# Optimization experiments

Measured on AMD Instinct MI355X. Metric: run time of the kernel, lower is better.

The kernel has to match this reference:

```python
import jax, jax.numpy as jnp
import numpy as np

EPS = 1e-8

def div_safe(n, d):
    return n / jnp.maximum(d, EPS)

def cos_sim(v1, v2):
    # torch F.cosine_similarity along last axis (broadcasting allowed)
    n1 = jnp.linalg.norm(v1, axis=-1)
    n2 = jnp.linalg.norm(v2, axis=-1)
    dot = jnp.sum(v1 * v2, axis=-1)
    return dot / (jnp.maximum(n1, EPS) * jnp.maximum(n2, EPS))

def cosine_pairwise(v1, v2):
    # v1: (B,L1,H), v2: (B,L2,H) -> (B,L1,L2)
    n1 = jnp.linalg.norm(v1, axis=2)[:, :, None]        # (B,L1,1)
    n2 = jnp.linalg.norm(v2, axis=2)[:, None, :]        # (B,1,L2)
    a = jnp.einsum('bih,bjh->bij', v1, v2)
    return div_safe(a, n1 * n2)

def mpm(v1, v2, w):
    # v1: (B,L,H); v2: (B,L,H) or (B,1,H) (broadcast); w: (P,H)
    mv1 = cos_sim(v1, v2)[..., None]                     # (B,L,1)
    v1w = w[None, None] * v1[:, :, None, :]              # (B,L,P,H)
    v2w = w[None, None] * v2[:, :, None, :]              # (B,L or 1,P,H)
    mvp = cos_sim(v1w, v2w)                              # (B,L,P)
    return [mv1, mvp]

def mpm_pairwise(v1, v2, w):
    # v1: (B,L1,H), v2: (B,L2,H), w: (P,H) -> (B,L1,L2,P)
    v1w = w[None, :, None, :] * v1[:, None, :, :]        # (B,P,L1,H)
    v2w = w[None, :, None, :] * v2[:, None, :, :]        # (B,P,L2,H)
    n = jnp.einsum('bpih,bpjh->bpij', v1w, v2w)
    n1 = jnp.linalg.norm(v1w, axis=3)[:, :, :, None]     # (B,P,L1,1)
    n2 = jnp.linalg.norm(v2w, axis=3)[:, :, None, :]     # (B,P,1,L2)
    return div_safe(n, n1 * n2).transpose(0, 2, 3, 1)

def matching_forward(context_p, mask_p, context_h, mask_h, params):
    H = params.shape[-1]
    B = context_p.shape[0]
    p_fw, p_bw = context_p[..., :H], context_p[..., H:]
    h_fw, h_bw = context_h[..., :H], context_h[..., H:]

    len_p = jnp.sum(mask_p, axis=1)
    len_h = jnp.sum(mask_h, axis=1)
    last_p = jnp.clip(len_p - 1, 0)
    last_h = jnp.clip(len_h - 1, 0)
    bidx = jnp.arange(B)
    p_fw_last = p_fw[bidx, last_p][:, None, :]           # (B,1,H)
    h_fw_last = h_fw[bidx, last_h][:, None, :]
    p_bw_last = p_bw[:, 0:1, :]
    h_bw_last = h_bw[:, 0:1, :]

    cos_fw = cosine_pairwise(p_fw, h_fw)                 # (B,L1,L2)
    cos_bw = cosine_pairwise(p_bw, h_bw)

    mv_p = [cos_fw.max(axis=2, keepdims=True), cos_fw.mean(axis=2, keepdims=True),
            cos_bw.max(axis=2, keepdims=True), cos_bw.mean(axis=2, keepdims=True)]
    mv_h = [cos_fw.max(axis=1)[..., None], cos_fw.mean(axis=1)[..., None],
            cos_bw.max(axis=1)[..., None], cos_bw.mean(axis=1)[..., None]]

    # full match
    mv_p += mpm(p_fw, h_fw_last, params[0]) + mpm(p_bw, h_bw_last, params[1])
    mv_h += mpm(h_fw, p_fw_last, params[0]) + mpm(h_bw, p_bw_last, params[1])

    # maxpool match
    m_fw = mpm_pairwise(p_fw, h_fw, params[2])           # (B,L1,L2,P)
    m_bw = mpm_pairwise(p_bw, h_bw, params[3])
    mv_p += [m_fw.max(axis=2), m_fw.mean(axis=2), m_bw.max(axis=2), m_bw.mean(axis=2)]
    mv_h += [m_fw.max(axis=1), m_fw.mean(axis=1), m_bw.max(axis=1), m_bw.mean(axis=1)]

    # attentive (mean) match -- sum over seq axis expressed as einsum, no 4D tensor
    att_mean_h_fw = div_safe(jnp.einsum('bij,bjh->bih', cos_fw, h_fw), cos_fw.sum(axis=2, keepdims=True))
    att_mean_h_bw = div_safe(jnp.einsum('bij,bjh->bih', cos_bw, h_bw), cos_bw.sum(axis=2, keepdims=True))
    att_mean_p_fw = div_safe(jnp.einsum('bij,bih->bjh', cos_fw, p_fw), cos_fw.sum(axis=1)[..., None])
    att_mean_p_bw = div_safe(jnp.einsum('bij,bih->bjh', cos_bw, p_bw), cos_bw.sum(axis=1)[..., None])
    mv_p += mpm(p_fw, att_mean_h_fw, params[4]) + mpm(p_bw, att_mean_h_bw, params[5])
    mv_h += mpm(h_fw, att_mean_p_fw, params[4]) + mpm(h_bw, att_mean_p_bw, params[5])

    # max-attentive match -- needs elementwise max over the pair axis
    att_max_h_fw = jnp.max(h_fw[:, None, :, :] * cos_fw[..., None], axis=2)  # (B,L1,H)
    att_max_h_bw = jnp.max(h_bw[:, None, :, :] * cos_bw[..., None], axis=2)
    att_max_p_fw = jnp.max(p_fw[:, :, None, :] * cos_fw[..., None], axis=1)  # (B,L2,H)
    att_max_p_bw = jnp.max(p_bw[:, :, None, :] * cos_bw[..., None], axis=1)
    mv_p += mpm(p_fw, att_max_h_fw, params[6]) + mpm(p_bw, att_max_h_bw, params[7])
    mv_h += mpm(h_fw, att_max_p_fw, params[6]) + mpm(h_bw, att_max_p_bw, params[7])

    return jnp.concatenate(mv_p, axis=2), jnp.concatenate(mv_h, axis=2)

def setup_inputs() -> dict:
    key = jax.random.key(0)
    k1, k2, k3 = jax.random.split(key, 3)
    B, L, H, P, M = 16, 128, 100, 20, 8
    context_p = jax.random.normal(k1, (B, L, 2 * H), dtype=jnp.float32)
    context_h = jax.random.normal(k2, (B, L, 2 * H), dtype=jnp.float32)
    mask_p = jnp.ones((B, L), dtype=jnp.int32)
    mask_h = jnp.ones((B, L), dtype=jnp.int32)
    # kaiming_normal_ (fan_in=H): std = sqrt(2/H)
    params = jax.random.normal(k3, (M, P, H), dtype=jnp.float32) * np.sqrt(2.0 / H)
    return {"context_p": context_p, "mask_p": mask_p,
            "context_h": context_h, "mask_h": mask_h, "params": params}

def reference(context_p, mask_p, context_h, mask_h, params):
    return matching_forward(context_p, mask_p, context_h, mask_h, params)
```

## Files before the change

kernel.cpp:

```cpp
#include <hip/hip_runtime.h>
#include <math.h>

#define B 16
#define L 128
#define H 100
#define P 20
#define CH 210
#define EPSF 1e-8f

#define OFF_COS    0u
#define OFF_COST   524288u
#define OFF_ROWSUM 1048576u
#define OFF_COLSUM 1052672u
#define OFF_LASTV  1056768u
#define OFF_W2T    1063168u
#define OFF_W2F    1079968u
#define OFF_NBUF   1101472u
#define OFF_ATT    1273504u

typedef __attribute__((ext_vector_type(8))) short bf16x8;
typedef __attribute__((ext_vector_type(4))) float f32x4;

__device__ inline unsigned short f2bf(float x) {
    union { float f; unsigned u; } c; c.f = x;
    unsigned r = c.u + 0x7fffu + ((c.u >> 16) & 1u);
    return (unsigned short)(r >> 16);
}

__global__ __launch_bounds__(128) void prep_kernel(
    const float* __restrict__ ctx_p, const int* __restrict__ mask_p,
    const float* __restrict__ ctx_h, const int* __restrict__ mask_h,
    float* __restrict__ lastv)
{
    const int b = blockIdx.x, is_h = blockIdx.y, t = threadIdx.x;
    const float* ctx = is_h ? ctx_h : ctx_p;
    const int* mask = is_h ? mask_h : mask_p;
    __shared__ int sm[L];
    sm[t] = mask[b*L + t];
    __syncthreads();
    for (int s = 64; s > 0; s >>= 1) {
        if (t < s) sm[t] += sm[t + s];
        __syncthreads();
    }
    int last = sm[0] - 1;
    if (last < 0) last = 0;
    if (t < H) {
        lastv[((size_t)(is_h*2 + 0)*B + b)*H + t] = ctx[(size_t)(b*L + last)*(2*H) + t];
        lastv[((size_t)(is_h*2 + 1)*B + b)*H + t] = ctx[(size_t)(b*L + 0)*(2*H) + H + t];
    }
}

__global__ __launch_bounds__(256) void wprep_kernel(
    const float* __restrict__ params, float* __restrict__ w2t, float* __restrict__ w2f)
{
    int e = blockIdx.x*256 + threadIdx.x;
    if (e < 8*25*4*21) {
        int m = e / 2100, r = e % 2100;
        int g = r / 84, q = r % 84, hh = q / 21, p = q % 21;
        int h = 4*g + hh;
        float v = 1.f;
        if (p < P) { float w = params[((size_t)m*P + p)*H + h]; v = w*w; }
        w2t[e] = v;
    }
    int e2 = e - 16800;
    if (e2 >= 0 && e2 < 8*21*128) {
        int m = e2 / (21*128), r = e2 % (21*128), p = r / 128, h = r % 128;
        float v = 0.f;
        if (h < H) {
            if (p < P) { float w = params[((size_t)m*P + p)*H + h]; v = w*w; }
            else v = 1.f;
        }
        w2f[e2] = v;
    }
}

__global__ __launch_bounds__(128) void norm_kernel(
    const float* __restrict__ ctx_p, const float* __restrict__ ctx_h,
    const float* __restrict__ w2t, float* __restrict__ nbuf)
{
    const int b = blockIdx.x, dir = blockIdx.y, side = blockIdx.z;
    const int i = threadIdx.x;
    const float* row = (side ? ctx_h : ctx_p) + (size_t)(b*L + i)*(2*H) + dir*H;
    const float* wt = w2t + (size_t)(2 + dir)*2100;
    float n2[21];
#pragma unroll
    for (int p = 0; p < 21; ++p) n2[p] = 0.f;
    for (int g = 0; g < 25; ++g) {
        float4 v = *(const float4*)(row + 4*g);
        float sq[4] = {v.x*v.x, v.y*v.y, v.z*v.z, v.w*v.w};
        const float* wg = wt + g*84;
#pragma unroll
        for (int hh = 0; hh < 4; ++hh)
#pragma unroll
            for (int p = 0; p < 21; ++p)
                n2[p] = fmaf(wg[hh*21 + p], sq[hh], n2[p]);
    }
    float* nb = nbuf + ((size_t)((dir*2 + side)*B + b)*21)*128;
#pragma unroll
    for (int p = 0; p < 21; ++p) nb[p*128 + i] = sqrtf(n2[p]);
}

__global__ __launch_bounds__(256, 2) void pair_kernel(
    const float* __restrict__ ctx_p, const float* __restrict__ ctx_h,
    const float* __restrict__ w2f, const float* __restrict__ nbuf,
    float* __restrict__ cosbuf, float* __restrict__ cosT,
    float* __restrict__ rowsum, float* __restrict__ colsum,
    float* __restrict__ out)
{
    const int b = blockIdx.x, dir = blockIdx.y, p = blockIdx.z;
    const int t = threadIdx.x;
    __shared__ short sB[2048*8];
    __shared__ float colred[2][4][128];

    for (int e = t; e < 2048; e += 256) {
        int cg = e >> 8, kt = (e >> 6) & 3, qq = (e >> 4) & 3, rl2 = e & 15;
        int row = cg*16 + rl2, kb = kt*32 + qq*8;
        float v[8];
#pragma unroll
        for (int j = 0; j < 8; ++j) v[j] = 0.f;
        const float* src = ctx_h + (size_t)(b*L + row)*(2*H) + dir*H;
        if (kb < H)     { float4 f = *(const float4*)(src + kb);     v[0]=f.x; v[1]=f.y; v[2]=f.z; v[3]=f.w; }
        if (kb + 4 < H) { float4 f = *(const float4*)(src + kb + 4); v[4]=f.x; v[5]=f.y; v[6]=f.z; v[7]=f.w; }
        bf16x8 pk;
#pragma unroll
        for (int j = 0; j < 8; ++j) pk[j] = (short)f2bf(v[j]);
        *(bf16x8*)&sB[e*8] = pk;
    }

    const int w = t >> 6, lane = t & 63, q = lane >> 4, rl = lane & 15;
    const float* w2row = w2f + ((size_t)(2 + dir)*21 + p)*128;
    bf16x8 af[2][4];
#pragma unroll
    for (int rgi = 0; rgi < 2; ++rgi) {
        int row = (w*2 + rgi)*16 + rl;
        const float* src = ctx_p + (size_t)(b*L + row)*(2*H) + dir*H;
#pragma unroll
        for (int kt = 0; kt < 4; ++kt) {
            int kb = kt*32 + q*8;
            float v[8];
#pragma unroll
            for (int j = 0; j < 8; ++j) v[j] = 0.f;
            if (kb < H) {
                float4 f = *(const float4*)(src + kb);
                float4 wv = *(const float4*)(w2row + kb);
                v[0]=f.x*wv.x; v[1]=f.y*wv.y; v[2]=f.z*wv.z; v[3]=f.w*wv.w;
            }
            if (kb + 4 < H) {
                float4 f = *(const float4*)(src + kb + 4);
                float4 wv = *(const float4*)(w2row + kb + 4);
                v[4]=f.x*wv.x; v[5]=f.y*wv.y; v[6]=f.z*wv.z; v[7]=f.w*wv.w;
            }
            bf16x8 pk;
#pragma unroll
            for (int j = 0; j < 8; ++j) pk[j] = (short)f2bf(v[j]);
            af[rgi][kt] = pk;
        }
    }
    __syncthreads();

    f32x4 acc[2][8];
#pragma unroll
    for (int rgi = 0; rgi < 2; ++rgi)
#pragma unroll
        for (int cg = 0; cg < 8; ++cg) acc[rgi][cg] = (f32x4)0.f;
#pragma unroll
    for (int kt = 0; kt < 4; ++kt) {
#pragma unroll
        for (int cg = 0; cg < 8; ++cg) {
            bf16x8 bfr = *(bf16x8*)&sB[((cg*4 + kt)*64 + lane)*8];
            acc[0][cg] = __builtin_amdgcn_mfma_f32_16x16x32_bf16(af[0][kt], bfr, acc[0][cg], 0, 0, 0);
            acc[1][cg] = __builtin_amdgcn_mfma_f32_16x16x32_bf16(af[1][kt], bfr, acc[1][cg], 0, 0, 0);
        }
    }

    const float* nbA = nbuf + (((size_t)(dir*2 + 0)*B + b)*21 + p)*128;
    const float* nbB = nbuf + (((size_t)(dir*2 + 1)*B + b)*21 + p)*128;
    float na[2][4];
#pragma unroll
    for (int rgi = 0; rgi < 2; ++rgi)
#pragma unroll
        for (int r = 0; r < 4; ++r) na[rgi][r] = nbA[(w*2 + rgi)*16 + q*4 + r];
    float nbv[8];
#pragma unroll
    for (int cg = 0; cg < 8; ++cg) nbv[cg] = nbB[cg*16 + rl];

    const bool iscos = (p == P);
    float* cosm  = cosbuf + (size_t)(dir*B + b)*16384;
    float* cosmT = cosT   + (size_t)(dir*B + b)*16384;

    int chmax, chmean;
    if (p < P) { chmax = (dir ? 86 : 46) + p; chmean = (dir ? 106 : 66) + p; }
    else       { chmax = dir*2;              chmean = dir*2 + 1; }

    float rowm[2][4], rows_[2][4], colm[8], cols_[8];
#pragma unroll
    for (int rgi = 0; rgi < 2; ++rgi)
#pragma unroll
        for (int r = 0; r < 4; ++r) { rowm[rgi][r] = -INFINITY; rows_[rgi][r] = 0.f; }
#pragma unroll
    for (int cg = 0; cg < 8; ++cg) { colm[cg] = -INFINITY; cols_[cg] = 0.f; }

#pragma unroll
    for (int rgi = 0; rgi < 2; ++rgi) {
        int i0 = (w*2 + rgi)*16 + q*4;
#pragma unroll
        for (int cg = 0; cg < 8; ++cg) {
            float m[4];
#pragma unroll
            for (int r = 0; r < 4; ++r) {
                float d = fmaxf(na[rgi][r]*nbv[cg], EPSF);
                m[r] = acc[rgi][cg][r] * __builtin_amdgcn_rcpf(d);
                rowm[rgi][r] = fmaxf(rowm[rgi][r], m[r]);
                rows_[rgi][r] += m[r];
            }
            float cM = fmaxf(fmaxf(m[0], m[1]), fmaxf(m[2], m[3]));
            colm[cg] = fmaxf(colm[cg], cM);
            cols_[cg] += (m[0] + m[1]) + (m[2] + m[3]);
            if (iscos) {
                int j = cg*16 + rl;
                float4 f4; f4.x = m[0]; f4.y = m[1]; f4.z = m[2]; f4.w = m[3];
                *(float4*)&cosmT[j*128 + i0] = f4;
#pragma unroll
                for (int r = 0; r < 4; ++r) cosm[(i0 + r)*128 + j] = m[r];
            }
        }
    }
#pragma unroll
    for (int rgi = 0; rgi < 2; ++rgi)
#pragma unroll
        for (int r = 0; r < 4; ++r) {
            float mx = rowm[rgi][r], sm = rows_[rgi][r];
#pragma unroll
            for (int d = 1; d < 16; d <<= 1) {
                mx = fmaxf(mx, __shfl_xor(mx, d));
                sm += __shfl_xor(sm, d);
            }
            if (rl == 0) {
                int i = (w*2 + rgi)*16 + q*4 + r;
                float* orow = out + (size_t)(b*L + i)*CH;
                orow[chmax] = mx; orow[chmean] = sm * (1.f/L);
                if (iscos) rowsum[(dir*B + b)*L + i] = sm;
            }
        }
#pragma unroll
    for (int cg = 0; cg < 8; ++cg) {
        float mx = colm[cg], sm = cols_[cg];
        mx = fmaxf(mx, __shfl_xor(mx, 16)); sm += __shfl_xor(sm, 16);
        mx = fmaxf(mx, __shfl_xor(mx, 32)); sm += __shfl_xor(sm, 32);
        if (q == 0) { colred[0][w][cg*16 + rl] = mx; colred[1][w][cg*16 + rl] = sm; }
    }
    __syncthreads();
    {
        int c = t & 127, kind = t >> 7;
        float v0 = colred[kind][0][c], v1 = colred[kind][1][c];
        float v2 = colred[kind][2][c], v3 = colred[kind][3][c];
        float* oh = out + (size_t)B*L*CH + (size_t)(b*L + c)*CH;
        if (kind == 0) {
            oh[chmax] = fmaxf(fmaxf(v0, v1), fmaxf(v2, v3));
        } else {
            float sm = (v0 + v1) + (v2 + v3);
            oh[chmean] = sm * (1.f/L);
            if (iscos) colsum[(dir*B + b)*L + c] = sm;
        }
    }
}

__global__ __launch_bounds__(256) void att_kernel(
    const float* __restrict__ ctx_p, const float* __restrict__ ctx_h,
    const float* __restrict__ cosbuf, const float* __restrict__ cosT,
    const float* __restrict__ rowsum, const float* __restrict__ colsum,
    float* __restrict__ attbuf)
{
    const int b = blockIdx.x;
    const int dir = blockIdx.y >> 1, side = blockIdx.y & 1;
    const int rc = blockIdx.z, r0 = rc*16;
    const int t = threadIdx.x;

    __shared__ float sv[L][H];
    __shared__ float cvT[L][16];

    const float* mat = (side ? cosbuf : cosT) + (size_t)(dir*B + b)*16384;
    const float* src = side ? ctx_p : ctx_h;

    for (int e = t; e < 3200; e += 256) {
        int row = e / 25, g = e - row*25;
        *(float4*)&sv[row][4*g] =
            *(const float4*)(src + (size_t)(b*L + row)*(2*H) + dir*H + 4*g);
    }
    for (int e = t; e < 2048; e += 256) {
        int s = e >> 4, r = e & 15;
        cvT[s][r] = mat[s*L + r0 + r];
    }
    __syncthreads();

    const int tr = t & 7, th = t >> 3;
    if (th < 25) {
        float acc[2][4], amx[2][4];
#pragma unroll
        for (int rr = 0; rr < 2; ++rr)
#pragma unroll
            for (int qq = 0; qq < 4; ++qq) { acc[rr][qq] = 0.f; amx[rr][qq] = -INFINITY; }
        for (int s = 0; s < L; ++s) {
            float2 c2 = *(const float2*)&cvT[s][2*tr];
            float4 v4 = *(const float4*)&sv[s][4*th];
            float cs[2] = {c2.x, c2.y};
            float vs[4] = {v4.x, v4.y, v4.z, v4.w};
#pragma unroll
            for (int rr = 0; rr < 2; ++rr)
#pragma unroll
                for (int qq = 0; qq < 4; ++qq) {
                    float pr = cs[rr] * vs[qq];
                    acc[rr][qq] += pr;
                    amx[rr][qq] = fmaxf(amx[rr][qq], pr);
                }
        }
        const float* den = side ? colsum : rowsum;
#pragma unroll
        for (int rr = 0; rr < 2; ++rr) {
            int rg = r0 + 2*tr + rr;
            float d = fmaxf(den[(dir*B + b)*L + rg], EPSF);
            float* meanp = attbuf + ((((size_t)side*2 + 0)*2 + dir)*B*L + (b*L + rg))*H + 4*th;
            float* maxp  = attbuf + ((((size_t)side*2 + 1)*2 + dir)*B*L + (b*L + rg))*H + 4*th;
            float4 fm; fm.x = acc[rr][0]/d; fm.y = acc[rr][1]/d; fm.z = acc[rr][2]/d; fm.w = acc[rr][3]/d;
            float4 fx; fx.x = amx[rr][0]; fx.y = amx[rr][1]; fx.z = amx[rr][2]; fx.w = amx[rr][3];
            *(float4*)meanp = fm;
            *(float4*)maxp  = fx;
        }
    }
}

__global__ __launch_bounds__(128) void point_kernel(
    const float* __restrict__ ctx_p, const float* __restrict__ ctx_h,
    const float* __restrict__ w2t,
    const float* __restrict__ lastv, const float* __restrict__ attbuf,
    float* __restrict__ out)
{
    const int b = blockIdx.x, side = blockIdx.y;
    const int m = blockIdx.z >> 1, ih = blockIdx.z & 1;
    const int t = threadIdx.x;
    const int il = t & 63, half = t >> 6;
    const int i = ih*64 + il;
    const int dir = m & 1;
    const int wsel_[6] = {0, 1, 4, 5, 6, 7};
    const int chb_[6]  = {4, 25, 126, 147, 168, 189};

    const float* v1p = (side ? ctx_h : ctx_p) + (size_t)(b*L + i)*(2*H) + dir*H;
    const float* v2p;
    if (m < 2) {
        v2p = lastv + ((size_t)((side ? 0 : 2) + dir)*B + b)*H;
    } else {
        int kind = (m >= 4) ? 1 : 0;
        v2p = attbuf + ((((size_t)side*2 + kind)*2 + dir)*B*L + (b*L + i))*H;
    }
    const float* wt = w2t + (size_t)wsel_[m]*2100;

    float s11[21], s22[21], s12[21];
#pragma unroll
    for (int p = 0; p < 21; ++p) { s11[p] = 0.f; s22[p] = 0.f; s12[p] = 0.f; }
    const int g0 = half ? 13 : 0, g1 = half ? 25 : 13;
    for (int g = g0; g < g1; ++g) {
        float4 x = *(const float4*)(v1p + 4*g);
        float4 y = *(const float4*)(v2p + 4*g);
        float xx[4] = {x.x*x.x, x.y*x.y, x.z*x.z, x.w*x.w};
        float yy[4] = {y.x*y.x, y.y*y.y, y.z*y.z, y.w*y.w};
        float xy[4] = {x.x*y.x, x.y*y.y, x.z*y.z, x.w*y.w};
        const float* wg = wt + g*84;
#pragma unroll
        for (int hh = 0; hh < 4; ++hh)
#pragma unroll
            for (int p = 0; p < 21; ++p) {
                float w2 = wg[hh*21 + p];
                s11[p] = fmaf(w2, xx[hh], s11[p]);
                s22[p] = fmaf(w2, yy[hh], s22[p]);
                s12[p] = fmaf(w2, xy[hh], s12[p]);
            }
    }
    __shared__ float red[3][21][64];
    if (half) {
#pragma unroll
        for (int p = 0; p < 21; ++p) {
            red[0][p][il] = s11[p]; red[1][p][il] = s22[p]; red[2][p][il] = s12[p];
        }
    }
    __syncthreads();
    if (!half) {
        float* orow = out + (size_t)side*B*L*CH + (size_t)(b*L + i)*CH;
#pragma unroll
        for (int p = 0; p < 21; ++p) {
            float a = s11[p] + red[0][p][il];
            float c = s22[p] + red[1][p][il];
            float d = s12[p] + red[2][p][il];
            float cv = d / (fmaxf(sqrtf(a), EPSF) * fmaxf(sqrtf(c), EPSF));
            orow[(p == P) ? chb_[m] : (chb_[m] + 1 + p)] = cv;
        }
    }
}

extern "C" void kernel_launch(void* const* d_in, const int* in_sizes, int n_in,
                              void* d_out, int out_size, void* d_ws, size_t ws_size,
                              hipStream_t stream) {
    const float* ctx_p  = (const float*)d_in[0];
    const int*   mask_p = (const int*)d_in[1];
    const float* ctx_h  = (const float*)d_in[2];
    const int*   mask_h = (const int*)d_in[3];
    const float* params = (const float*)d_in[4];
    float* out = (float*)d_out;

    float* ws = (float*)d_ws;
    float* cosbuf = ws + OFF_COS;
    float* cosT   = ws + OFF_COST;
    float* rowsum = ws + OFF_ROWSUM;
    float* colsum = ws + OFF_COLSUM;
    float* lastv  = ws + OFF_LASTV;
    float* w2t    = ws + OFF_W2T;
    float* w2f    = ws + OFF_W2F;
    float* nbuf   = ws + OFF_NBUF;
    float* attbuf = ws + OFF_ATT;

    prep_kernel <<<dim3(B, 2),     128, 0, stream>>>(ctx_p, mask_p, ctx_h, mask_h, lastv);
    wprep_kernel<<<dim3(150),      256, 0, stream>>>(params, w2t, w2f);
    norm_kernel <<<dim3(B, 2, 2),  128, 0, stream>>>(ctx_p, ctx_h, w2t, nbuf);
    pair_kernel <<<dim3(B, 2, 21), 256, 0, stream>>>(ctx_p, ctx_h, w2f, nbuf,
                                                     cosbuf, cosT, rowsum, colsum, out);
    att_kernel  <<<dim3(B, 4, 8),  256, 0, stream>>>(ctx_p, ctx_h, cosbuf, cosT,
                                                     rowsum, colsum, attbuf);
    point_kernel<<<dim3(B, 2, 12), 128, 0, stream>>>(ctx_p, ctx_h, w2t, lastv, attbuf, out);
}
```

Before: 148.8 us.

## Fuse prep, weight-prep and norm kernels into pair kernel

Removes three small preliminary launches. Their work now runs inside the pair kernel: extra blocks build w2t and the last-token vectors, and each pair block computes its own weighted row norms into LDS straight from params. This cuts launch overhead and the serial dependency chain, plus the w2f and nbuf round trips through global memory. In exchange the norm work is repeated per block, adding a 100-element loop per thread before the MFMA stage.

```diff
diff --git a/kernel.cpp b/kernel.cpp
--- a/kernel.cpp
+++ b/kernel.cpp
@@ -14,9 +14,7 @@
 #define OFF_COLSUM 1052672u
 #define OFF_LASTV  1056768u
 #define OFF_W2T    1063168u
-#define OFF_W2F    1079968u
-#define OFF_NBUF   1101472u
-#define OFF_ATT    1273504u
+#define OFF_ATT    1079968u
 
 typedef __attribute__((ext_vector_type(8))) short bf16x8;
 typedef __attribute__((ext_vector_type(4))) float f32x4;
@@ -27,94 +25,57 @@
     return (unsigned short)(r >> 16);
 }
 
-__global__ __launch_bounds__(128) void prep_kernel(
-    const float* __restrict__ ctx_p, const int* __restrict__ mask_p,
-    const float* __restrict__ ctx_h, const int* __restrict__ mask_h,
-    float* __restrict__ lastv)
-{
-    const int b = blockIdx.x, is_h = blockIdx.y, t = threadIdx.x;
-    const float* ctx = is_h ? ctx_h : ctx_p;
-    const int* mask = is_h ? mask_h : mask_p;
-    __shared__ int sm[L];
-    sm[t] = mask[b*L + t];
-    __syncthreads();
-    for (int s = 64; s > 0; s >>= 1) {
-        if (t < s) sm[t] += sm[t + s];
-        __syncthreads();
-    }
-    int last = sm[0] - 1;
-    if (last < 0) last = 0;
-    if (t < H) {
-        lastv[((size_t)(is_h*2 + 0)*B + b)*H + t] = ctx[(size_t)(b*L + last)*(2*H) + t];
-        lastv[((size_t)(is_h*2 + 1)*B + b)*H + t] = ctx[(size_t)(b*L + 0)*(2*H) + H + t];
-    }
-}
-
-__global__ __launch_bounds__(256) void wprep_kernel(
-    const float* __restrict__ params, float* __restrict__ w2t, float* __restrict__ w2f)
-{
-    int e = blockIdx.x*256 + threadIdx.x;
-    if (e < 8*25*4*21) {
-        int m = e / 2100, r = e % 2100;
-        int g = r / 84, q = r % 84, hh = q / 21, p = q % 21;
-        int h = 4*g + hh;
-        float v = 1.f;
-        if (p < P) { float w = params[((size_t)m*P + p)*H + h]; v = w*w; }
-        w2t[e] = v;
-    }
-    int e2 = e - 16800;
-    if (e2 >= 0 && e2 < 8*21*128) {
-        int m = e2 / (21*128), r = e2 % (21*128), p = r / 128, h = r % 128;
-        float v = 0.f;
-        if (h < H) {
-            if (p < P) { float w = params[((size_t)m*P + p)*H + h]; v = w*w; }
-            else v = 1.f;
-        }
-        w2f[e2] = v;
-    }
-}
-
-__global__ __launch_bounds__(128) void norm_kernel(
-    const float* __restrict__ ctx_p, const float* __restrict__ ctx_h,
-    const float* __restrict__ w2t, float* __restrict__ nbuf)
-{
-    const int b = blockIdx.x, dir = blockIdx.y, side = blockIdx.z;
-    const int i = threadIdx.x;
-    const float* row = (side ? ctx_h : ctx_p) + (size_t)(b*L + i)*(2*H) + dir*H;
-    const float* wt = w2t + (size_t)(2 + dir)*2100;
-    float n2[21];
-#pragma unroll
-    for (int p = 0; p < 21; ++p) n2[p] = 0.f;
-    for (int g = 0; g < 25; ++g) {
-        float4 v = *(const float4*)(row + 4*g);
-        float sq[4] = {v.x*v.x, v.y*v.y, v.z*v.z, v.w*v.w};
-        const float* wg = wt + g*84;
-#pragma unroll
-        for (int hh = 0; hh < 4; ++hh)
-#pragma unroll
-            for (int p = 0; p < 21; ++p)
-                n2[p] = fmaf(wg[hh*21 + p], sq[hh], n2[p]);
-    }
-    float* nb = nbuf + ((size_t)((dir*2 + side)*B + b)*21)*128;
-#pragma unroll
-    for (int p = 0; p < 21; ++p) nb[p*128 + i] = sqrtf(n2[p]);
-}
-
 __global__ __launch_bounds__(256, 2) void pair_kernel(
     const float* __restrict__ ctx_p, const float* __restrict__ ctx_h,
-    const float* __restrict__ w2f, const float* __restrict__ nbuf,
+    const int* __restrict__ mask_p, const int* __restrict__ mask_h,
+    const float* __restrict__ params,
     float* __restrict__ cosbuf, float* __restrict__ cosT,
     float* __restrict__ rowsum, float* __restrict__ colsum,
+    float* __restrict__ lastv, float* __restrict__ w2t,
     float* __restrict__ out)
 {
-    const int b = blockIdx.x, dir = blockIdx.y, p = blockIdx.z;
-    const int t = threadIdx.x;
-    __shared__ short sB[2048*8];
-    __shared__ float colred[2][4][128];
+    __shared__ __align__(16) char smem[37888];
+    const int k = blockIdx.x, t = threadIdx.x;
+
+    if (k >= 672) {
+        if (k == 672) {
+            for (int e = t; e < 16800; e += 256) {
+                int m = e / 2100, r = e % 2100;
+                int g = r / 84, qq = r % 84, hh = qq / 21, p = qq % 21;
+                int h = 4*g + hh;
+                float v = 1.f;
+                if (p < P) { float w = params[((size_t)m*P + p)*H + h]; v = w*w; }
+                w2t[e] = v;
+            }
+        } else {
+            const int task = k - 673, b = task >> 1, is_h = task & 1;
+            const float* ctx = is_h ? ctx_h : ctx_p;
+            const int* mask = is_h ? mask_h : mask_p;
+            int* sm = (int*)smem;
+            if (t < 128) sm[t] = mask[b*L + t];
+            __syncthreads();
+            for (int s = 64; s > 0; s >>= 1) {
+                if (t < s) sm[t] += sm[t + s];
+                __syncthreads();
+            }
+            int last = sm[0] - 1;
+            if (last < 0) last = 0;
+            if (t < H) {
+                lastv[((size_t)(is_h*2 + 0)*B + b)*H + t] = ctx[(size_t)(b*L + last)*(2*H) + t];
+                lastv[((size_t)(is_h*2 + 1)*B + b)*H + t] = ctx[(size_t)(b*L + 0)*(2*H) + H + t];
+            }
+        }
+        return;
+    }
+
+    const int b = k & 15, dir = (k >> 4) & 1, p = k >> 5;
+    short* sB     = (short*)smem;
+    float* colred = (float*)(smem + 32768);
+    float* nlds   = (float*)(smem + 32768 + 4096);
 
     for (int e = t; e < 2048; e += 256) {
-        int cg = e >> 8, kt = (e >> 6) & 3, qq = (e >> 4) & 3, rl2 = e & 15;
-        int row = cg*16 + rl2, kb = kt*32 + qq*8;
+        int cgi = e >> 8, kt = (e >> 6) & 3, qq = (e >> 4) & 3, rl2 = e & 15;
+        int row = cgi*16 + rl2, kb = kt*32 + qq*8;
         float v[8];
 #pragma unroll
         for (int j = 0; j < 8; ++j) v[j] = 0.f;
@@ -127,8 +88,9 @@
         *(bf16x8*)&sB[e*8] = pk;
     }
 
+    const float* prow = params + ((size_t)(2 + dir)*P + p)*H;
+
     const int w = t >> 6, lane = t & 63, q = lane >> 4, rl = lane & 15;
-    const float* w2row = w2f + ((size_t)(2 + dir)*21 + p)*128;
     bf16x8 af[2][4];
 #pragma unroll
     for (int rgi = 0; rgi < 2; ++rgi) {
@@ -140,15 +102,20 @@
             float v[8];
 #pragma unroll
             for (int j = 0; j < 8; ++j) v[j] = 0.f;
-            if (kb < H) {
-                float4 f = *(const float4*)(src + kb);
-                float4 wv = *(const float4*)(w2row + kb);
-                v[0]=f.x*wv.x; v[1]=f.y*wv.y; v[2]=f.z*wv.z; v[3]=f.w*wv.w;
-            }
-            if (kb + 4 < H) {
-                float4 f = *(const float4*)(src + kb + 4);
-                float4 wv = *(const float4*)(w2row + kb + 4);
-                v[4]=f.x*wv.x; v[5]=f.y*wv.y; v[6]=f.z*wv.z; v[7]=f.w*wv.w;
+            if (p < P) {
+                if (kb < H) {
+                    float4 f = *(const float4*)(src + kb);
+                    float4 wv = *(const float4*)(prow + kb);
+                    v[0]=f.x*wv.x*wv.x; v[1]=f.y*wv.y*wv.y; v[2]=f.z*wv.z*wv.z; v[3]=f.w*wv.w*wv.w;
+                }
+                if (kb + 4 < H) {
+                    float4 f = *(const float4*)(src + kb + 4);
+                    float4 wv = *(const float4*)(prow + kb + 4);
+                    v[4]=f.x*wv.x*wv.x; v[5]=f.y*wv.y*wv.y; v[6]=f.z*wv.z*wv.z; v[7]=f.w*wv.w*wv.w;
+                }
+            } else {
+                if (kb < H)     { float4 f = *(const float4*)(src + kb);     v[0]=f.x; v[1]=f.y; v[2]=f.z; v[3]=f.w; }
+                if (kb + 4 < H) { float4 f = *(const float4*)(src + kb + 4); v[4]=f.x; v[5]=f.y; v[6]=f.z; v[7]=f.w; }
             }
             bf16x8 pk;
 #pragma unroll
@@ -156,33 +123,54 @@
             af[rgi][kt] = pk;
         }
     }
+
+    {
+        const int r = t & 127, sd = t >> 7;
+        const float* nrow = (sd ? ctx_h : ctx_p) + (size_t)(b*L + r)*(2*H) + dir*H;
+        float n2 = 0.f;
+        if (p < P) {
+            for (int g = 0; g < 25; ++g) {
+                float4 v = *(const float4*)(nrow + 4*g);
+                float4 wv = *(const float4*)(prow + 4*g);
+                n2 = fmaf(wv.x*wv.x, v.x*v.x, n2);
+                n2 = fmaf(wv.y*wv.y, v.y*v.y, n2);
+                n2 = fmaf(wv.z*wv.z, v.z*v.z, n2);
+                n2 = fmaf(wv.w*wv.w, v.w*v.w, n2);
+            }
+        } else {
+            for (int g = 0; g < 25; ++g) {
+                float4 v = *(const float4*)(nrow + 4*g);
+                n2 = fmaf(v.x, v.x, n2); n2 = fmaf(v.y, v.y, n2);
+                n2 = fmaf(v.z, v.z, n2); n2 = fmaf(v.w, v.w, n2);
+            }
+        }
+        nlds[sd*128 + r] = sqrtf(n2);
+    }
     __syncthreads();
 
     f32x4 acc[2][8];
 #pragma unroll
     for (int rgi = 0; rgi < 2; ++rgi)
 #pragma unroll
-        for (int cg = 0; cg < 8; ++cg) acc[rgi][cg] = (f32x4)0.f;
+        for (int cgi = 0; cgi < 8; ++cgi) acc[rgi][cgi] = (f32x4)0.f;
 #pragma unroll
     for (int kt = 0; kt < 4; ++kt) {
 #pragma unroll
-        for (int cg = 0; cg < 8; ++cg) {
-            bf16x8 bfr = *(bf16x8*)&sB[((cg*4 + kt)*64 + lane)*8];
-            acc[0][cg] = __builtin_amdgcn_mfma_f32_16x16x32_bf16(af[0][kt], bfr, acc[0][cg], 0, 0, 0);
-            acc[1][cg] = __builtin_amdgcn_mfma_f32_16x16x32_bf16(af[1][kt], bfr, acc[1][cg], 0, 0, 0);
-        }
-    }
-
-    const float* nbA = nbuf + (((size_t)(dir*2 + 0)*B + b)*21 + p)*128;
-    const float* nbB = nbuf + (((size_t)(dir*2 + 1)*B + b)*21 + p)*128;
+        for (int cgi = 0; cgi < 8; ++cgi) {
+            bf16x8 bfr = *(bf16x8*)&sB[((cgi*4 + kt)*64 + lane)*8];
+            acc[0][cgi] = __builtin_amdgcn_mfma_f32_16x16x32_bf16(af[0][kt], bfr, acc[0][cgi], 0, 0, 0);
+            acc[1][cgi] = __builtin_amdgcn_mfma_f32_16x16x32_bf16(af[1][kt], bfr, acc[1][cgi], 0, 0, 0);
+        }
+    }
+
     float na[2][4];
 #pragma unroll
     for (int rgi = 0; rgi < 2; ++rgi)
 #pragma unroll
-        for (int r = 0; r < 4; ++r) na[rgi][r] = nbA[(w*2 + rgi)*16 + q*4 + r];
+        for (int r = 0; r < 4; ++r) na[rgi][r] = nlds[0*128 + (w*2 + rgi)*16 + q*4 + r];
     float nbv[8];
 #pragma unroll
-    for (int cg = 0; cg < 8; ++cg) nbv[cg] = nbB[cg*16 + rl];
+    for (int cgi = 0; cgi < 8; ++cgi) nbv[cgi] = nlds[1*128 + cgi*16 + rl];
 
     const bool iscos = (p == P);
     float* cosm  = cosbuf + (size_t)(dir*B + b)*16384;
@@ -198,26 +186,26 @@
 #pragma unroll
         for (int r = 0; r < 4; ++r) { rowm[rgi][r] = -INFINITY; rows_[rgi][r] = 0.f; }
 #pragma unroll
-    for (int cg = 0; cg < 8; ++cg) { colm[cg] = -INFINITY; cols_[cg] = 0.f; }
+    for (int cgi = 0; cgi < 8; ++cgi) { colm[cgi] = -INFINITY; cols_[cgi] = 0.f; }
 
 #pragma unroll
     for (int rgi = 0; rgi < 2; ++rgi) {
         int i0 = (w*2 + rgi)*16 + q*4;
 #pragma unroll
-        for (int cg = 0; cg < 8; ++cg) {
+        for (int cgi = 0; cgi < 8; ++cgi) {
             float m[4];
 #pragma unroll
             for (int r = 0; r < 4; ++r) {
-                float d = fmaxf(na[rgi][r]*nbv[cg], EPSF);
-                m[r] = acc[rgi][cg][r] * __builtin_amdgcn_rcpf(d);
+                float d = fmaxf(na[rgi][r]*nbv[cgi], EPSF);
+                m[r] = acc[rgi][cgi][r] * __builtin_amdgcn_rcpf(d);
                 rowm[rgi][r] = fmaxf(rowm[rgi][r], m[r]);
                 rows_[rgi][r] += m[r];
             }
             float cM = fmaxf(fmaxf(m[0], m[1]), fmaxf(m[2], m[3]));
-            colm[cg] = fmaxf(colm[cg], cM);
-            cols_[cg] += (m[0] + m[1]) + (m[2] + m[3]);
+            colm[cgi] = fmaxf(colm[cgi], cM);
+            cols_[cgi] += (m[0] + m[1]) + (m[2] + m[3]);
             if (iscos) {
-                int j = cg*16 + rl;
+                int j = cgi*16 + rl;
                 float4 f4; f4.x = m[0]; f4.y = m[1]; f4.z = m[2]; f4.w = m[3];
                 *(float4*)&cosmT[j*128 + i0] = f4;
 #pragma unroll
@@ -243,17 +231,20 @@
             }
         }
 #pragma unroll
-    for (int cg = 0; cg < 8; ++cg) {
-        float mx = colm[cg], sm = cols_[cg];
+    for (int cgi = 0; cgi < 8; ++cgi) {
+        float mx = colm[cgi], sm = cols_[cgi];
         mx = fmaxf(mx, __shfl_xor(mx, 16)); sm += __shfl_xor(sm, 16);
         mx = fmaxf(mx, __shfl_xor(mx, 32)); sm += __shfl_xor(sm, 32);
-        if (q == 0) { colred[0][w][cg*16 + rl] = mx; colred[1][w][cg*16 + rl] = sm; }
+        if (q == 0) {
+            colred[(0*4 + w)*128 + cgi*16 + rl] = mx;
+            colred[(1*4 + w)*128 + cgi*16 + rl] = sm;
+        }
     }
     __syncthreads();
     {
         int c = t & 127, kind = t >> 7;
-        float v0 = colred[kind][0][c], v1 = colred[kind][1][c];
-        float v2 = colred[kind][2][c], v3 = colred[kind][3][c];
+        float v0 = colred[(kind*4 + 0)*128 + c], v1 = colred[(kind*4 + 1)*128 + c];
+        float v2 = colred[(kind*4 + 2)*128 + c], v3 = colred[(kind*4 + 3)*128 + c];
         float* oh = out + (size_t)B*L*CH + (size_t)(b*L + c)*CH;
         if (kind == 0) {
             oh[chmax] = fmaxf(fmaxf(v0, v1), fmaxf(v2, v3));
@@ -413,15 +404,11 @@
     float* colsum = ws + OFF_COLSUM;
     float* lastv  = ws + OFF_LASTV;
     float* w2t    = ws + OFF_W2T;
-    float* w2f    = ws + OFF_W2F;
-    float* nbuf   = ws + OFF_NBUF;
     float* attbuf = ws + OFF_ATT;
 
-    prep_kernel <<<dim3(B, 2),     128, 0, stream>>>(ctx_p, mask_p, ctx_h, mask_h, lastv);
-    wprep_kernel<<<dim3(150),      256, 0, stream>>>(params, w2t, w2f);
-    norm_kernel <<<dim3(B, 2, 2),  128, 0, stream>>>(ctx_p, ctx_h, w2t, nbuf);
-    pair_kernel <<<dim3(B, 2, 21), 256, 0, stream>>>(ctx_p, ctx_h, w2f, nbuf,
-                                                     cosbuf, cosT, rowsum, colsum, out);
+    pair_kernel <<<dim3(705),      256, 0, stream>>>(ctx_p, ctx_h, mask_p, mask_h, params,
+                                                     cosbuf, cosT, rowsum, colsum,
+                                                     lastv, w2t, out);
     att_kernel  <<<dim3(B, 4, 8),  256, 0, stream>>>(ctx_p, ctx_h, cosbuf, cosT,
                                                      rowsum, colsum, attbuf);
     point_kernel<<<dim3(B, 2, 12), 128, 0, stream>>>(ctx_p, ctx_h, w2t, lastv, attbuf, out);
```

Result: faster. 135.1 us (-9.2%).
